# Performance work log

Measured on AMD Instinct MI355X. Metric: run time of the kernel, lower is better.

Reference implementation:

```python
import jax, jax.numpy as jnp
import numpy as np

B, M, K, F_IN, H = 64, 1024, 16, 4, 64  # B graphs of M nodes each, k=16 neighbors


def _knn_idx(h):
    # h: [B, M, H] -> indices of K nearest neighbors (excluding self): [B, M, K]
    sq = jnp.sum(h * h, axis=-1)                                   # [B, M]
    d = sq[:, :, None] + sq[:, None, :] - 2.0 * jnp.einsum('bmf,bnf->bmn', h, h)
    d = jnp.where(jnp.eye(M, dtype=bool)[None], jnp.float32(jnp.inf), d)
    _, idx = jax.lax.top_k(-d, K)                                  # smallest distances
    return idx


def _edge_conv(h, w1, b1, w2, b2):
    # Dynamic-graph EdgeConv with max aggregation (PyG default):
    # msg = MLP(concat[x_i, x_j - x_i]); out_i = max_j msg
    idx = _knn_idx(h)                                              # [B, M, K]
    x_j = jax.vmap(lambda hb, ib: hb[ib])(h, idx)                  # [B, M, K, H]
    x_i = jnp.broadcast_to(h[:, :, None, :], x_j.shape)
    msg = jnp.concatenate([x_i, x_j - x_i], axis=-1)               # [B, M, K, 2H]
    msg = jax.nn.relu(msg @ w1 + b1) @ w2 + b2                     # [B, M, K, H]
    return jnp.max(msg, axis=2)                                    # [B, M, H]


def setup_inputs() -> dict:
    key = jax.random.key(0)
    ks = jax.random.split(key, 20)

    def lin(k, fi, fo):
        return jax.random.normal(k, (fi, fo), jnp.float32) / np.sqrt(fi)

    inp = {
        'x': jax.random.normal(ks[0], (B * M, F_IN), jnp.float32),
        'batch': jnp.repeat(jnp.arange(B, dtype=jnp.int64), M),
        # encoder: Linear(4,32) ReLU Linear(32,64) ReLU
        'enc_w1': lin(ks[1], F_IN, 32), 'enc_b1': jnp.zeros((32,), jnp.float32),
        'enc_w2': lin(ks[2], 32, H),    'enc_b2': jnp.zeros((H,), jnp.float32),
        # EdgeConv MLPs: Linear(128,64) ReLU Linear(64,64)
        'ec1_w1': lin(ks[3], 2 * H, H), 'ec1_b1': jnp.zeros((H,), jnp.float32),
        'ec1_w2': lin(ks[4], H, H),     'ec1_b2': jnp.zeros((H,), jnp.float32),
        'ec2_w1': lin(ks[5], 2 * H, H), 'ec2_b1': jnp.zeros((H,), jnp.float32),
        'ec2_w2': lin(ks[6], H, H),     'ec2_b2': jnp.zeros((H,), jnp.float32),
        # output MLP: Linear(64,32) ReLU Linear(32,1)
        'out_w1': lin(ks[7], H, 32),    'out_b1': jnp.zeros((32,), jnp.float32),
        'out_w2': lin(ks[8], 32, 1),    'out_b2': jnp.zeros((1,), jnp.float32),
    }
    return inp


def reference(x, batch, enc_w1, enc_b1, enc_w2, enc_b2,
              ec1_w1, ec1_b1, ec1_w2, ec1_b2,
              ec2_w1, ec2_b1, ec2_w2, ec2_b2,
              out_w1, out_b1, out_w2, out_b2):
    # batch is repeat(arange(B), M): equal-size graphs -> reshape into [B, M, .]
    h = jax.nn.relu(jax.nn.relu(x @ enc_w1 + enc_b1) @ enc_w2 + enc_b2)  # [N, 64]
    h = h.reshape(B, M, H)
    h = _edge_conv(h, ec1_w1, ec1_b1, ec1_w2, ec1_b2)
    h = _edge_conv(h, ec2_w1, ec2_b1, ec2_w2, ec2_b2)
    g = jnp.mean(h, axis=1)                                        # global_mean_pool -> [B, 64]
    out = jax.nn.relu(g @ out_w1 + out_b1) @ out_w2 + out_b2       # [B, 1]
    return out.reshape(-1)                                         # [B]
```

## Files before the change

### kernel.cpp

```cpp
#include <hip/hip_runtime.h>
#include <math.h>

#define B_ 64
#define M_ 1024
#define H_ 64
#define N_ (B_*M_)

typedef _Float16 half8 __attribute__((ext_vector_type(8)));
typedef float  floatx4 __attribute__((ext_vector_type(4)));

#define MFMA16(a,b,c) __builtin_amdgcn_mfma_f32_16x16x32_f16(a,b,c,0,0,0)
#define MED3(a,b,c)   __builtin_amdgcn_fmed3f(a,b,c)

__global__ __launch_bounds__(256) void enc_kernel(
    const float* __restrict__ x,
    const float* __restrict__ w1,
    const float* __restrict__ b1,
    const float* __restrict__ w2,
    const float* __restrict__ b2,
    const float* __restrict__ ecw1,
    _Float16* __restrict__ hhi,
    _Float16* __restrict__ hlo,
    float* __restrict__ sq,
    float* __restrict__ A)
{
    __shared__ float sw1[4*32];
    __shared__ float sb1[32];
    __shared__ float sw2[32*64];
    __shared__ float sb2[64];
    __shared__ float swb[64*64];
    int t = threadIdx.x;
    for (int i = t; i < 128; i += 256) sw1[i] = w1[i];
    if (t < 32) sb1[t] = b1[t];
    for (int i = t; i < 2048; i += 256) sw2[i] = w2[i];
    if (t < 64) sb2[t] = b2[t];
    for (int i = t; i < 4096; i += 256) swb[i] = ecw1[4096 + i];
    __syncthreads();
    int n = blockIdx.x * 256 + t;
    float4 xv = *(const float4*)(x + (size_t)n*4);
    float hid[32];
    #pragma unroll
    for (int o = 0; o < 32; ++o) {
        float a = sb1[o] + xv.x*sw1[0*32+o] + xv.y*sw1[1*32+o]
                        + xv.z*sw1[2*32+o] + xv.w*sw1[3*32+o];
        hid[o] = fmaxf(a, 0.f);
    }
    float4 hv[16];
    float sqa = 0.f;
    #pragma unroll 4
    for (int oc = 0; oc < 16; ++oc) {
        float4 acc = make_float4(sb2[oc*4+0], sb2[oc*4+1], sb2[oc*4+2], sb2[oc*4+3]);
        #pragma unroll
        for (int f = 0; f < 32; ++f) {
            float4 w = *(const float4*)(sw2 + f*64 + oc*4);
            float hv_ = hid[f];
            acc.x += hv_*w.x; acc.y += hv_*w.y; acc.z += hv_*w.z; acc.w += hv_*w.w;
        }
        acc.x = fmaxf(acc.x,0.f); acc.y = fmaxf(acc.y,0.f);
        acc.z = fmaxf(acc.z,0.f); acc.w = fmaxf(acc.w,0.f);
        hv[oc] = acc;
        sqa += acc.x*acc.x + acc.y*acc.y + acc.z*acc.z + acc.w*acc.w;
        union { _Float16 f[4]; uint2 u; } Hh, Hl;
        Hh.f[0]=(_Float16)acc.x; Hh.f[1]=(_Float16)acc.y;
        Hh.f[2]=(_Float16)acc.z; Hh.f[3]=(_Float16)acc.w;
        Hl.f[0]=(_Float16)(acc.x-(float)Hh.f[0]); Hl.f[1]=(_Float16)(acc.y-(float)Hh.f[1]);
        Hl.f[2]=(_Float16)(acc.z-(float)Hh.f[2]); Hl.f[3]=(_Float16)(acc.w-(float)Hh.f[3]);
        *(uint2*)(hhi + (size_t)n*64 + oc*4) = Hh.u;
        *(uint2*)(hlo + (size_t)n*64 + oc*4) = Hl.u;
    }
    sq[n] = sqa;
    float* dst = A + (size_t)n*64;
    #pragma unroll 2
    for (int oc = 0; oc < 16; ++oc) {
        float4 acc = make_float4(0.f,0.f,0.f,0.f);
        #pragma unroll
        for (int f = 0; f < 64; ++f) {
            float xf = ((const float*)hv)[f];
            float4 w = *(const float4*)(swb + f*64 + oc*4);
            acc.x += xf*w.x; acc.y += xf*w.y; acc.z += xf*w.z; acc.w += xf*w.w;
        }
        *(float4*)(dst + oc*4) = acc;
    }
}

__global__ __launch_bounds__(256) void prep2_kernel(
    const _Float16* __restrict__ hhi,
    const _Float16* __restrict__ hlo,
    const float* __restrict__ ecw1,
    float* __restrict__ A,
    float* __restrict__ sq)
{
    __shared__ float swb[64*64];
    int t = threadIdx.x;
    for (int i = t; i < 4096; i += 256) swb[i] = ecw1[4096 + i];
    __syncthreads();
    int n = blockIdx.x * 256 + t;
    float hv[64];
    const _Float16* sh = hhi + (size_t)n*64;
    const _Float16* sl = hlo + (size_t)n*64;
    float sqa = 0.f;
    #pragma unroll
    for (int c = 0; c < 8; ++c) {
        half8 a = *(const half8*)(sh + c*8);
        half8 b = *(const half8*)(sl + c*8);
        #pragma unroll
        for (int j = 0; j < 8; ++j) {
            float v = (float)a[j] + (float)b[j];
            hv[c*8+j] = v;
            sqa += v*v;
        }
    }
    sq[n] = sqa;
    float* dst = A + (size_t)n*64;
    #pragma unroll 2
    for (int oc = 0; oc < 16; ++oc) {
        float4 acc = make_float4(0.f,0.f,0.f,0.f);
        #pragma unroll
        for (int f = 0; f < 64; ++f) {
            float xf = hv[f];
            float4 w = *(const float4*)(swb + f*64 + oc*4);
            acc.x += xf*w.x; acc.y += xf*w.y; acc.z += xf*w.z; acc.w += xf*w.w;
        }
        *(float4*)(dst + oc*4) = acc;
    }
}

__global__ __launch_bounds__(256) void knn_kernel(
    const _Float16* __restrict__ hhi,
    const _Float16* __restrict__ hlo,
    const float* __restrict__ sqg,
    unsigned short* __restrict__ knn)
{
    __shared__ float D[4][64*33];
    __shared__ float sqS[1024];
    int t = threadIdx.x, lane = t & 63, w = t >> 6;
    int bi = blockIdx.x;
    int g  = (bi & 7) | ((bi >> 7) << 3);
    int qt = (bi >> 3) & 15;
    const _Float16* hhig = hhi + (size_t)g*M_*64;
    const _Float16* hlog = hlo + (size_t)g*M_*64;
    const float*    sqb  = sqg + (size_t)g*M_;
    ((float4*)sqS)[t] = ((const float4*)sqb)[t];

    int m16  = lane & 15;
    int koct = (lane >> 4) * 8;
    int crow = (lane >> 4) * 4;
    half8 Ahi[4][2], Alo[4][2];
    #pragma unroll
    for (int rb = 0; rb < 4; ++rb) {
        const _Float16* ph = hhig + (size_t)(qt*64 + rb*16 + m16)*64;
        const _Float16* pl = hlog + (size_t)(qt*64 + rb*16 + m16)*64;
        Ahi[rb][0] = *(const half8*)(ph + koct);
        Ahi[rb][1] = *(const half8*)(ph + 32 + koct);
        Alo[rb][0] = *(const half8*)(pl + koct);
        Alo[rb][1] = *(const half8*)(pl + 32 + koct);
    }
    #pragma unroll
    for (int rb = 0; rb < 4; ++rb)
        #pragma unroll
        for (int p = 0; p < 2; ++p)
            #pragma unroll
            for (int j = 0; j < 8; ++j) {
                Ahi[rb][p][j] = Ahi[rb][p][j] * (_Float16)-2.0f;
                Alo[rb][p][j] = Alo[rb][p][j] * (_Float16)-2.0f;
            }
    __syncthreads();
    float c1r[4][4];
    #pragma unroll
    for (int rb = 0; rb < 4; ++rb)
        #pragma unroll
        for (int r = 0; r < 4; ++r)
            c1r[rb][r] = 1.f + sqS[qt*64 + rb*16 + crow + r];

    float* Dw = D[w];
    float bd[16];
    #pragma unroll
    for (int k = 0; k < 16; ++k) bd[k] = INFINITY;
    int cand0 = w*256;
    int selfc_all = qt*64 + lane;

    #pragma unroll
    for (int cc = 0; cc < 8; ++cc) {
        int cbase = cand0 + cc*32;
        half8 Bhi[2][2], Blo[2][2];
        #pragma unroll
        for (int cb = 0; cb < 2; ++cb) {
            const _Float16* ph = hhig + (size_t)(cbase + cb*16 + m16)*64;
            const _Float16* pl = hlog + (size_t)(cbase + cb*16 + m16)*64;
            Bhi[cb][0] = *(const half8*)(ph + koct);
            Bhi[cb][1] = *(const half8*)(ph + 32 + koct);
            Blo[cb][0] = *(const half8*)(pl + koct);
            Blo[cb][1] = *(const half8*)(pl + 32 + koct);
        }
        #pragma unroll
        for (int rb = 0; rb < 4; ++rb) {
            #pragma unroll
            for (int cb = 0; cb < 2; ++cb) {
                float sqj = sqS[cbase + cb*16 + m16];
                floatx4 acc = {c1r[rb][0]+sqj, c1r[rb][1]+sqj,
                               c1r[rb][2]+sqj, c1r[rb][3]+sqj};
                acc = MFMA16(Ahi[rb][0], Bhi[cb][0], acc);
                acc = MFMA16(Ahi[rb][1], Bhi[cb][1], acc);
                acc = MFMA16(Ahi[rb][0], Blo[cb][0], acc);
                acc = MFMA16(Ahi[rb][1], Blo[cb][1], acc);
                acc = MFMA16(Alo[rb][0], Bhi[cb][0], acc);
                acc = MFMA16(Alo[rb][1], Bhi[cb][1], acc);
                #pragma unroll
                for (int r = 0; r < 4; ++r)
                    Dw[(rb*16 + crow + r)*33 + cb*16 + m16] = acc[r];
            }
        }
        const float* drow = Dw + lane*33;
        int selfc = selfc_all - cbase;
        #pragma unroll
        for (int c8 = 0; c8 < 4; ++c8) {
            float sv[8];
            #pragma unroll
            for (int j = 0; j < 8; ++j) sv[j] = drow[c8*8 + j];
            #pragma unroll
            for (int j = 0; j < 8; ++j) {
                int c = c8*8 + j;
                unsigned kb = (__float_as_uint(sv[j]) & 0xFFFFFC00u)
                            | (unsigned)(cbase + c);
                float fk = __uint_as_float(kb);
                if (c == selfc) fk = INFINITY;
                float nb0 = fminf(bd[0], fk);
                #pragma unroll
                for (int k = 15; k >= 1; --k) bd[k] = MED3(fk, bd[k-1], bd[k]);
                bd[0] = nb0;
            }
        }
    }

    __syncthreads();
    float* md = &D[0][0];
    #pragma unroll
    for (int k = 0; k < 16; ++k) md[lane*65 + w*16 + k] = bd[k];
    __syncthreads();
    if (w == 0) {
        float b2[16];
        #pragma unroll
        for (int k = 0; k < 16; ++k) b2[k] = INFINITY;
        const float* mrow = md + lane*65;
        #pragma unroll
        for (int c8 = 0; c8 < 8; ++c8) {
            float sv[8];
            #pragma unroll
            for (int j = 0; j < 8; ++j) sv[j] = mrow[c8*8 + j];
            #pragma unroll
            for (int j = 0; j < 8; ++j) {
                float s = sv[j];
                float nb0 = fminf(b2[0], s);
                #pragma unroll
                for (int k = 15; k >= 1; --k) b2[k] = MED3(s, b2[k-1], b2[k]);
                b2[0] = nb0;
            }
        }
        union { unsigned short us[16]; uint4 v4[2]; } o;
        #pragma unroll
        for (int k = 0; k < 16; ++k)
            o.us[k] = (unsigned short)(__float_as_uint(b2[k]) & 1023u);
        size_t gq = (size_t)g*M_ + qt*64 + lane;
        uint4* dst = (uint4*)(knn + gq*16);
        dst[0] = o.v4[0];
        dst[1] = o.v4[1];
    }
}

__global__ __launch_bounds__(256) void edge_kernel(
    _Float16* __restrict__ hhi,
    _Float16* __restrict__ hlo,
    const float* __restrict__ A,
    const unsigned short* __restrict__ knn,
    const float* __restrict__ w1,
    const float* __restrict__ b1,
    const float* __restrict__ w2,
    const float* __restrict__ b2)
{
    __shared__ __align__(16) _Float16 wdf[16*64*8];
    __shared__ __align__(16) _Float16 w2f[16*64*8];
    float* CsB = (float*)w2f;
    int t = threadIdx.x;
    for (int u = t; u < 512; u += 256) {
        int ulane = u & 63, nt = u >> 7, ks = (u >> 6) & 1;
        int n = nt*16 + (ulane & 15);
        int kbase = ks*32 + ((ulane >> 4) * 8);
        int fh = (((nt*2+ks)*2+0)*64 + ulane)*8;
        int fl = (((nt*2+ks)*2+1)*64 + ulane)*8;
        #pragma unroll
        for (int j = 0; j < 8; ++j) {
            int k = kbase + j;
            float vd = w1[k*64+n] - w1[4096 + k*64+n];
            _Float16 dh = (_Float16)vd;
            wdf[fh+j] = dh;
            wdf[fl+j] = (_Float16)(vd - (float)dh);
            float v2 = w2[k*64+n];
            _Float16 h2 = (_Float16)v2;
            w2f[fh+j] = h2;
            w2f[fl+j] = (_Float16)(v2 - (float)h2);
        }
    }
    __syncthreads();
    int lane = t & 63, wid = t >> 6;
    int m16 = lane & 15, gid = lane >> 4;
    int koct = gid*8, crow = gid*4;
    int bi = blockIdx.x;
    int g  = (bi & 7) | ((bi >> 7) << 3);
    int qt = (bi >> 3) & 15;
    int i0 = g*M_ + qt*64 + wid*16;
    const float* Ab = A + (size_t)g*M_*H_;

    half8 W2r[4][2][2];
    #pragma unroll
    for (int nt = 0; nt < 4; ++nt)
        #pragma unroll
        for (int ks = 0; ks < 2; ++ks)
            #pragma unroll
            for (int p = 0; p < 2; ++p)
                W2r[nt][ks][p] = *(const half8*)&w2f[(((nt*2+ks)*2+p)*64+lane)*8];

    float b1v[4];
    #pragma unroll
    for (int nt = 0; nt < 4; ++nt) b1v[nt] = b1[nt*16+m16];
    float b2v = b2[gid*16+m16];
    __syncthreads();

    half8 Hh[2], Hl[2];
    #pragma unroll
    for (int ks = 0; ks < 2; ++ks) {
        Hh[ks] = *(const half8*)(hhi + (size_t)(i0+m16)*64 + ks*32 + koct);
        Hl[ks] = *(const half8*)(hlo + (size_t)(i0+m16)*64 + ks*32 + koct);
    }
    #pragma unroll
    for (int nt = 0; nt < 4; ++nt) {
        floatx4 acc = {b1v[nt], b1v[nt], b1v[nt], b1v[nt]};
        #pragma unroll
        for (int ks = 0; ks < 2; ++ks) {
            half8 wh = *(const half8*)&wdf[(((nt*2+ks)*2+0)*64+lane)*8];
            half8 wl = *(const half8*)&wdf[(((nt*2+ks)*2+1)*64+lane)*8];
            acc = MFMA16(Hh[ks], wh, acc);
            acc = MFMA16(Hh[ks], wl, acc);
            acc = MFMA16(Hl[ks], wh, acc);
        }
        #pragma unroll
        for (int r = 0; r < 4; ++r)
            CsB[((wid*16) + crow + r)*64 + nt*16 + m16] = acc[r];
    }
    __syncthreads();

    const unsigned short* knb = knn + (size_t)i0*16;
    #pragma unroll 2
    for (int nn = 0; nn < 16; ++nn) {
        int j = knb[nn*16 + m16];
        const float* Ap = Ab + (size_t)j*64;
        half8 Mh[2], Ml[2];
        #pragma unroll
        for (int ks = 0; ks < 2; ++ks) {
            float4 a0 = *(const float4*)(Ap + ks*32 + koct);
            float4 a1 = *(const float4*)(Ap + ks*32 + koct + 4);
            const float* cp = &CsB[(wid*16 + nn)*64 + ks*32 + koct];
            float4 c0 = *(const float4*)cp;
            float4 c1 = *(const float4*)(cp+4);
            float mv[8] = {
                fmaxf(a0.x+c0.x,0.f), fmaxf(a0.y+c0.y,0.f),
                fmaxf(a0.z+c0.z,0.f), fmaxf(a0.w+c0.w,0.f),
                fmaxf(a1.x+c1.x,0.f), fmaxf(a1.y+c1.y,0.f),
                fmaxf(a1.z+c1.z,0.f), fmaxf(a1.w+c1.w,0.f)};
            #pragma unroll
            for (int jj = 0; jj < 8; ++jj) {
                _Float16 hi = (_Float16)mv[jj];
                Mh[ks][jj] = hi;
                Ml[ks][jj] = (_Float16)(mv[jj]-(float)hi);
            }
        }
        floatx4 acc[4];
        #pragma unroll
        for (int nt = 0; nt < 4; ++nt) {
            acc[nt] = (floatx4){0.f,0.f,0.f,0.f};
            #pragma unroll
            for (int ks = 0; ks < 2; ++ks) {
                acc[nt] = MFMA16(Mh[ks], W2r[nt][ks][0], acc[nt]);
                acc[nt] = MFMA16(Mh[ks], W2r[nt][ks][1], acc[nt]);
                acc[nt] = MFMA16(Ml[ks], W2r[nt][ks][0], acc[nt]);
            }
        }
        float om[4];
        #pragma unroll
        for (int nt = 0; nt < 4; ++nt) {
            float mr = fmaxf(fmaxf(acc[nt][0], acc[nt][1]),
                             fmaxf(acc[nt][2], acc[nt][3]));
            mr = fmaxf(mr, __shfl_xor(mr, 16, 64));
            mr = fmaxf(mr, __shfl_xor(mr, 32, 64));
            om[nt] = mr;
        }
        float val = (gid == 0) ? om[0] : (gid == 1) ? om[1]
                  : (gid == 2) ? om[2] : om[3];
        float ov = val + b2v;
        _Float16 oh = (_Float16)ov;
        _Float16 ol = (_Float16)(ov - (float)oh);
        hhi[(size_t)(i0+nn)*64 + lane] = oh;
        hlo[(size_t)(i0+nn)*64 + lane] = ol;
    }
}

__global__ __launch_bounds__(256) void pool_kernel(
    const _Float16* __restrict__ hhi,
    const _Float16* __restrict__ hlo,
    const float* __restrict__ w1,
    const float* __restrict__ b1,
    const float* __restrict__ w2,
    const float* __restrict__ b2,
    float* __restrict__ out)
{
    __shared__ float part[4][64];
    __shared__ float g[64];
    __shared__ float hid[32];
    int t = threadIdx.x;
    int o = t & 63, p = t >> 6;
    int b = blockIdx.x;
    const _Float16* hb = hhi + (size_t)b*M_*H_;
    const _Float16* lb = hlo + (size_t)b*M_*H_;
    float s = 0.f;
    for (int m = p; m < M_; m += 4)
        s += (float)hb[(size_t)m*64 + o] + (float)lb[(size_t)m*64 + o];
    part[p][o] = s;
    __syncthreads();
    if (t < 64) g[t] = (part[0][t] + part[1][t] + part[2][t] + part[3][t]) * (1.f/M_);
    __syncthreads();
    if (t < 32) {
        float a = b1[t];
        for (int f = 0; f < 64; ++f) a += g[f] * w1[f*32 + t];
        hid[t] = fmaxf(a, 0.f);
    }
    __syncthreads();
    if (t == 0) {
        float a = b2[0];
        for (int f = 0; f < 32; ++f) a += hid[f] * w2[f];
        out[b] = a;
    }
}

extern "C" void kernel_launch(void* const* d_in, const int* in_sizes, int n_in,
                              void* d_out, int out_size, void* d_ws, size_t ws_size,
                              hipStream_t stream)
{
    (void)in_sizes; (void)n_in; (void)out_size; (void)ws_size;
    const float* x      = (const float*)d_in[0];
    const float* enc_w1 = (const float*)d_in[2];
    const float* enc_b1 = (const float*)d_in[3];
    const float* enc_w2 = (const float*)d_in[4];
    const float* enc_b2 = (const float*)d_in[5];
    const float* ec1_w1 = (const float*)d_in[6];
    const float* ec1_b1 = (const float*)d_in[7];
    const float* ec1_w2 = (const float*)d_in[8];
    const float* ec1_b2 = (const float*)d_in[9];
    const float* ec2_w1 = (const float*)d_in[10];
    const float* ec2_b1 = (const float*)d_in[11];
    const float* ec2_w2 = (const float*)d_in[12];
    const float* ec2_b2 = (const float*)d_in[13];
    const float* out_w1 = (const float*)d_in[14];
    const float* out_b1 = (const float*)d_in[15];
    const float* out_w2 = (const float*)d_in[16];
    const float* out_b2 = (const float*)d_in[17];

    char* ws = (char*)d_ws;
    _Float16*       hhi = (_Float16*)(ws);
    _Float16*       hlo = (_Float16*)(ws + (size_t)N_*64*2);
    float*          A   = (float*)   (ws + (size_t)N_*64*4);
    unsigned short* idx = (unsigned short*)(ws + (size_t)N_*64*8);
    float*          sq  = (float*)   (ws + (size_t)N_*64*8 + (size_t)N_*16*2);

    enc_kernel<<<N_/256, 256, 0, stream>>>(x, enc_w1, enc_b1, enc_w2, enc_b2,
                                           ec1_w1, hhi, hlo, sq, A);
    knn_kernel <<<B_*16, 256, 0, stream>>>(hhi, hlo, sq, idx);
    edge_kernel<<<N_/64, 256, 0, stream>>>(hhi, hlo, A, idx,
                                           ec1_w1, ec1_b1, ec1_w2, ec1_b2);
    prep2_kernel<<<N_/256, 256, 0, stream>>>(hhi, hlo, ec2_w1, A, sq);
    knn_kernel <<<B_*16, 256, 0, stream>>>(hhi, hlo, sq, idx);
    edge_kernel<<<N_/64, 256, 0, stream>>>(hhi, hlo, A, idx,
                                           ec2_w1, ec2_b1, ec2_w2, ec2_b2);
    pool_kernel<<<B_, 256, 0, stream>>>(hhi, hlo, out_w1, out_b1, out_w2, out_b2,
                                        (float*)d_out);
}
```

Before: 425.9 us.

## Restructure kNN so each wave scans all candidates for 16 queries, merge via shuffles

The kNN kernel previously had each wave compute a 64x256 distance tile into LDS, read rows back per lane, and then merge four per-wave top-16 lists in LDS using a single wave. Now each wave owns 16 queries and streams all 1024 candidates 16 at a time with MFMA. The four lanes that share a query each keep a partial top-16 from the accumulator registers, and these are merged with xor shuffles and a bitonic min-merge. This removes the LDS distance buffer, the LDS round trip and the serial one-wave final merge. Separately, the edge kernel now prefetches the neighbor indices into registers before the first MLP stage, which adds register pressure in exchange for hiding that load latency.

```diff
diff --git a/kernel.cpp b/kernel.cpp
--- a/kernel.cpp
+++ b/kernel.cpp
@@ -131,7 +131,6 @@
     const float* __restrict__ sqg,
     unsigned short* __restrict__ knn)
 {
-    __shared__ float D[4][64*33];
     __shared__ float sqS[1024];
     int t = threadIdx.x, lane = t & 63, w = t >> 6;
     int bi = blockIdx.x;
@@ -142,125 +141,93 @@
     const float*    sqb  = sqg + (size_t)g*M_;
     ((float4*)sqS)[t] = ((const float4*)sqb)[t];
 
-    int m16  = lane & 15;
-    int koct = (lane >> 4) * 8;
-    int crow = (lane >> 4) * 4;
-    half8 Ahi[4][2], Alo[4][2];
-    #pragma unroll
-    for (int rb = 0; rb < 4; ++rb) {
-        const _Float16* ph = hhig + (size_t)(qt*64 + rb*16 + m16)*64;
-        const _Float16* pl = hlog + (size_t)(qt*64 + rb*16 + m16)*64;
-        Ahi[rb][0] = *(const half8*)(ph + koct);
-        Ahi[rb][1] = *(const half8*)(ph + 32 + koct);
-        Alo[rb][0] = *(const half8*)(pl + koct);
-        Alo[rb][1] = *(const half8*)(pl + 32 + koct);
-    }
-    #pragma unroll
-    for (int rb = 0; rb < 4; ++rb)
+    int m16 = lane & 15;
+    int gid = lane >> 4;
+    int koct = gid * 8;
+    int qloc = qt*64 + w*16 + m16;
+
+    half8 Bqh[2], Bql[2];
+    {
+        const _Float16* qh = hhig + (size_t)qloc*64;
+        const _Float16* ql = hlog + (size_t)qloc*64;
+        Bqh[0] = *(const half8*)(qh + koct);
+        Bqh[1] = *(const half8*)(qh + 32 + koct);
+        Bql[0] = *(const half8*)(ql + koct);
+        Bql[1] = *(const half8*)(ql + 32 + koct);
         #pragma unroll
         for (int p = 0; p < 2; ++p)
             #pragma unroll
             for (int j = 0; j < 8; ++j) {
-                Ahi[rb][p][j] = Ahi[rb][p][j] * (_Float16)-2.0f;
-                Alo[rb][p][j] = Alo[rb][p][j] * (_Float16)-2.0f;
+                Bqh[p][j] = Bqh[p][j] * (_Float16)-2.0f;
+                Bql[p][j] = Bql[p][j] * (_Float16)-2.0f;
             }
-    __syncthreads();
-    float c1r[4][4];
-    #pragma unroll
-    for (int rb = 0; rb < 4; ++rb)
-        #pragma unroll
-        for (int r = 0; r < 4; ++r)
-            c1r[rb][r] = 1.f + sqS[qt*64 + rb*16 + crow + r];
-
-    float* Dw = D[w];
+    }
+    __syncthreads();
+    float c1q = 1.f + sqS[qloc];
+
     float bd[16];
     #pragma unroll
     for (int k = 0; k < 16; ++k) bd[k] = INFINITY;
-    int cand0 = w*256;
-    int selfc_all = qt*64 + lane;
-
-    #pragma unroll
-    for (int cc = 0; cc < 8; ++cc) {
-        int cbase = cand0 + cc*32;
-        half8 Bhi[2][2], Blo[2][2];
-        #pragma unroll
-        for (int cb = 0; cb < 2; ++cb) {
-            const _Float16* ph = hhig + (size_t)(cbase + cb*16 + m16)*64;
-            const _Float16* pl = hlog + (size_t)(cbase + cb*16 + m16)*64;
-            Bhi[cb][0] = *(const half8*)(ph + koct);
-            Bhi[cb][1] = *(const half8*)(ph + 32 + koct);
-            Blo[cb][0] = *(const half8*)(pl + koct);
-            Blo[cb][1] = *(const half8*)(pl + 32 + koct);
-        }
-        #pragma unroll
-        for (int rb = 0; rb < 4; ++rb) {
-            #pragma unroll
-            for (int cb = 0; cb < 2; ++cb) {
-                float sqj = sqS[cbase + cb*16 + m16];
-                floatx4 acc = {c1r[rb][0]+sqj, c1r[rb][1]+sqj,
-                               c1r[rb][2]+sqj, c1r[rb][3]+sqj};
-                acc = MFMA16(Ahi[rb][0], Bhi[cb][0], acc);
-                acc = MFMA16(Ahi[rb][1], Bhi[cb][1], acc);
-                acc = MFMA16(Ahi[rb][0], Blo[cb][0], acc);
-                acc = MFMA16(Ahi[rb][1], Blo[cb][1], acc);
-                acc = MFMA16(Alo[rb][0], Bhi[cb][0], acc);
-                acc = MFMA16(Alo[rb][1], Bhi[cb][1], acc);
-                #pragma unroll
-                for (int r = 0; r < 4; ++r)
-                    Dw[(rb*16 + crow + r)*33 + cb*16 + m16] = acc[r];
+
+    #pragma unroll 4
+    for (int ct = 0; ct < 64; ++ct) {
+        int c0 = ct*16;
+        const _Float16* ph = hhig + (size_t)(c0 + m16)*64;
+        const _Float16* pl = hlog + (size_t)(c0 + m16)*64;
+        half8 Ah0 = *(const half8*)(ph + koct);
+        half8 Ah1 = *(const half8*)(ph + 32 + koct);
+        half8 Al0 = *(const half8*)(pl + koct);
+        half8 Al1 = *(const half8*)(pl + 32 + koct);
+        float4 sqc = *(const float4*)(sqS + c0 + gid*4);
+        floatx4 acc = {c1q + sqc.x, c1q + sqc.y, c1q + sqc.z, c1q + sqc.w};
+        acc = MFMA16(Ah0, Bqh[0], acc);
+        acc = MFMA16(Ah1, Bqh[1], acc);
+        acc = MFMA16(Ah0, Bql[0], acc);
+        acc = MFMA16(Ah1, Bql[1], acc);
+        acc = MFMA16(Al0, Bqh[0], acc);
+        acc = MFMA16(Al1, Bqh[1], acc);
+        #pragma unroll
+        for (int r = 0; r < 4; ++r) {
+            int cand = c0 + gid*4 + r;
+            unsigned kb = (__float_as_uint(acc[r]) & 0xFFFFFC00u) | (unsigned)cand;
+            float fk = __uint_as_float(kb);
+            if (cand == qloc) fk = INFINITY;
+            float nb0 = fminf(bd[0], fk);
+            #pragma unroll
+            for (int k = 15; k >= 1; --k) bd[k] = MED3(fk, bd[k-1], bd[k]);
+            bd[0] = nb0;
+        }
+    }
+
+    #pragma unroll
+    for (int X = 16; X <= 32; X <<= 1) {
+        float nb[16];
+        #pragma unroll
+        for (int k = 0; k < 16; ++k) {
+            float ov = __shfl_xor(bd[15-k], X, 64);
+            nb[k] = fminf(bd[k], ov);
+        }
+        #pragma unroll
+        for (int d = 8; d >= 1; d >>= 1) {
+            #pragma unroll
+            for (int i = 0; i < 16; ++i) {
+                if (!(i & d)) {
+                    float lo = fminf(nb[i], nb[i+d]);
+                    float hi = fmaxf(nb[i], nb[i+d]);
+                    nb[i] = lo; nb[i+d] = hi;
+                }
             }
         }
-        const float* drow = Dw + lane*33;
-        int selfc = selfc_all - cbase;
-        #pragma unroll
-        for (int c8 = 0; c8 < 4; ++c8) {
-            float sv[8];
-            #pragma unroll
-            for (int j = 0; j < 8; ++j) sv[j] = drow[c8*8 + j];
-            #pragma unroll
-            for (int j = 0; j < 8; ++j) {
-                int c = c8*8 + j;
-                unsigned kb = (__float_as_uint(sv[j]) & 0xFFFFFC00u)
-                            | (unsigned)(cbase + c);
-                float fk = __uint_as_float(kb);
-                if (c == selfc) fk = INFINITY;
-                float nb0 = fminf(bd[0], fk);
-                #pragma unroll
-                for (int k = 15; k >= 1; --k) bd[k] = MED3(fk, bd[k-1], bd[k]);
-                bd[0] = nb0;
-            }
-        }
-    }
-
-    __syncthreads();
-    float* md = &D[0][0];
-    #pragma unroll
-    for (int k = 0; k < 16; ++k) md[lane*65 + w*16 + k] = bd[k];
-    __syncthreads();
-    if (w == 0) {
-        float b2[16];
-        #pragma unroll
-        for (int k = 0; k < 16; ++k) b2[k] = INFINITY;
-        const float* mrow = md + lane*65;
-        #pragma unroll
-        for (int c8 = 0; c8 < 8; ++c8) {
-            float sv[8];
-            #pragma unroll
-            for (int j = 0; j < 8; ++j) sv[j] = mrow[c8*8 + j];
-            #pragma unroll
-            for (int j = 0; j < 8; ++j) {
-                float s = sv[j];
-                float nb0 = fminf(b2[0], s);
-                #pragma unroll
-                for (int k = 15; k >= 1; --k) b2[k] = MED3(s, b2[k-1], b2[k]);
-                b2[0] = nb0;
-            }
-        }
+        #pragma unroll
+        for (int k = 0; k < 16; ++k) bd[k] = nb[k];
+    }
+
+    if (lane < 16) {
         union { unsigned short us[16]; uint4 v4[2]; } o;
         #pragma unroll
         for (int k = 0; k < 16; ++k)
-            o.us[k] = (unsigned short)(__float_as_uint(b2[k]) & 1023u);
-        size_t gq = (size_t)g*M_ + qt*64 + lane;
+            o.us[k] = (unsigned short)(__float_as_uint(bd[k]) & 1023u);
+        size_t gq = (size_t)g*M_ + qt*64 + w*16 + lane;
         uint4* dst = (uint4*)(knn + gq*16);
         dst[0] = o.v4[0];
         dst[1] = o.v4[1];
@@ -331,6 +298,11 @@
         Hh[ks] = *(const half8*)(hhi + (size_t)(i0+m16)*64 + ks*32 + koct);
         Hl[ks] = *(const half8*)(hlo + (size_t)(i0+m16)*64 + ks*32 + koct);
     }
+    const unsigned short* knb = knn + (size_t)i0*16;
+    int kidx[16];
+    #pragma unroll
+    for (int nn = 0; nn < 16; ++nn) kidx[nn] = knb[nn*16 + m16];
+
     #pragma unroll
     for (int nt = 0; nt < 4; ++nt) {
         floatx4 acc = {b1v[nt], b1v[nt], b1v[nt], b1v[nt]};
@@ -348,11 +320,9 @@
     }
     __syncthreads();
 
-    const unsigned short* knb = knn + (size_t)i0*16;
     #pragma unroll 2
     for (int nn = 0; nn < 16; ++nn) {
-        int j = knb[nn*16 + m16];
-        const float* Ap = Ab + (size_t)j*64;
+        const float* Ap = Ab + (size_t)kidx[nn]*64;
         half8 Mh[2], Ml[2];
         #pragma unroll
         for (int ks = 0; ks < 2; ++ks) {
```

Measured after the change: 549.8 us. +29.1%, slower.
